# Kernel tuning notes

Measured on AMD Instinct MI355X. Metric: run time of the kernel, lower is better.

Reference implementation:

```python
import jax, jax.numpy as jnp
import numpy as np

HIDDEN = 1024
B, S = 4, 2048


def setup_inputs() -> dict:
    key = jax.random.key(0)
    ks = jax.random.split(key, 9)
    scale = 1.0 / np.sqrt(HIDDEN)
    mk = lambda k: (jax.random.normal(k, (HIDDEN, HIDDEN), dtype=jnp.float32) * scale)
    return {
        "x": jax.random.normal(ks[0], (B, S, HIDDEN), dtype=jnp.float32),
        "Wq": mk(ks[1]), "bq": jnp.zeros((HIDDEN,), jnp.float32),
        "Wk": mk(ks[2]), "bk": jnp.zeros((HIDDEN,), jnp.float32),
        "Wv": mk(ks[3]), "bv": jnp.zeros((HIDDEN,), jnp.float32),
        "Wo": mk(ks[4]), "bo": jnp.zeros((HIDDEN,), jnp.float32),
    }


def reference(x, Wq, bq, Wk, bk, Wv, bv, Wo, bo):
    # Single-head attention over the full hidden dim (num_heads unused in source).
    # Linear(H,H): y = x @ W^T + b ; weights stored [out,in] torch-style.
    q = jnp.einsum("bsh,oh->bso", x, Wq) + bq  # [B,S,H]
    k = jnp.einsum("bsh,oh->bso", x, Wk) + bk
    v = jnp.einsum("bsh,oh->bso", x, Wv) + bv
    scores = jnp.einsum("bqh,bkh->bqk", q, k) / jnp.sqrt(jnp.float32(HIDDEN))
    attn = jax.nn.softmax(scores, axis=-1)  # dropout rate is 0.0 (eval-equivalent)
    ctx = jnp.einsum("bqk,bkh->bqh", attn, v)
    return jnp.einsum("bsh,oh->bso", ctx, Wo) + bo
```

## Files before the change

### kernel.cpp

```cpp
#include <hip/hip_runtime.h>

#define HID 1024
#define SEQ 2048
#define NB 4
#define BS 8192

typedef __attribute__((ext_vector_type(8))) short short8;
typedef __attribute__((ext_vector_type(8))) unsigned short ushort8;
typedef __attribute__((ext_vector_type(4))) float f32x4;

__device__ __forceinline__ float bf2f(unsigned short u) {
  unsigned int x = ((unsigned int)u) << 16;
  return __builtin_bit_cast(float, x);
}
__device__ __forceinline__ unsigned short f2bf(float f) {
  unsigned int x = __builtin_bit_cast(unsigned int, f);
  x = x + 0x7fffu + ((x >> 16) & 1u);
  return (unsigned short)(x >> 16);
}

#define GLOAD16(g, l)                                                          \
  __builtin_amdgcn_global_load_lds(                                            \
      (const __attribute__((address_space(1))) unsigned int*)(g),              \
      (__attribute__((address_space(3))) unsigned int*)(l), 16, 0, 0)

__global__ void cast_f32_to_bf16(const float* __restrict__ in,
                                 unsigned short* __restrict__ out, int n) {
  int i = (blockIdx.x * 256 + threadIdx.x) * 8;
  if (i >= n) return;
  f32x4 a = *(const f32x4*)(in + i);
  f32x4 b = *(const f32x4*)(in + i + 4);
  ushort8 o;
  o[0] = f2bf(a[0]); o[1] = f2bf(a[1]); o[2] = f2bf(a[2]); o[3] = f2bf(a[3]);
  o[4] = f2bf(b[0]); o[5] = f2bf(b[1]); o[6] = f2bf(b[2]); o[7] = f2bf(b[3]);
  *(ushort8*)(out + i) = o;
}

__global__ __launch_bounds__(256) void transpose_cast(
    const float* __restrict__ in, unsigned short* __restrict__ out) {
  __shared__ float t[32][33];
  const int bx = blockIdx.x * 32, by = blockIdx.y * 32;
  const int tx = threadIdx.x & 31, ty = threadIdx.x >> 5;
#pragma unroll
  for (int i = 0; i < 4; ++i)
    t[ty + i * 8][tx] = in[(by + ty + i * 8) * 1024 + bx + tx];
  __syncthreads();
#pragma unroll
  for (int i = 0; i < 4; ++i)
    out[(bx + ty + i * 8) * 1024 + by + tx] = f2bf(t[tx][ty + i * 8]);
}

__global__ __launch_bounds__(256) void bias_fuse(const float* __restrict__ Wo,
                                                 const float* __restrict__ bv,
                                                 const float* __restrict__ bo,
                                                 float* __restrict__ bp) {
  const int row = blockIdx.x * 4 + (threadIdx.x >> 6);
  const int lane = threadIdx.x & 63;
  float s = 0.f;
  for (int k = lane; k < 1024; k += 64) s += Wo[row * 1024 + k] * bv[k];
#pragma unroll
  for (int off = 32; off >= 1; off >>= 1) s += __shfl_xor(s, off, 64);
  if (lane == 0) bp[row] = s + bo[row];
}

template <int BN, int OUT_F32, int BIAS_MODE, int EPI>
__global__ __launch_bounds__(256, 3) void gemm_tlp(
    const unsigned short* __restrict__ A, const unsigned short* __restrict__ B,
    void* __restrict__ Cv, const float* __restrict__ bias,
    const float* __restrict__ bias2, float* __restrict__ Srow, int K, int lda,
    int ldb, int ldc, long long bsA, long long bsB, long long bsC,
    float alpha) {
  static_assert(BN == 128 || BN == 64, "BN");
  constexpr int NF = BN / 32;
  constexpr int CB = BN / 64;

  __shared__ unsigned short lA[2][128 * 32];
  __shared__ unsigned short lB[2][BN * 32];

  const int tid = threadIdx.x;
  const int lane = tid & 63, wid = tid >> 6;
  const int fr = lane & 15, fq = lane >> 4;
  const int wm = wid >> 1, wn = wid & 1;

  const int nx = gridDim.x;
  const int nwg = nx * gridDim.y;
  int f = blockIdx.y * nx + blockIdx.x;
  f = (f & 7) * (nwg >> 3) + (f >> 3);
  const int bx = f % nx, by = f / nx;
  const int bz = blockIdx.z;

  const unsigned short* Ag = A + bz * bsA + (long long)by * 128 * lda;
  const unsigned short* Bg = B + bz * bsB + (long long)bx * BN * ldb;
  const int NT = K >> 5;

  const int srow = tid >> 2;
  const int scol = 8 * ((tid & 3) ^ ((tid >> 4) & 3));
  const int lbase = wid * 512;

  auto stageA = [&](int t) {
    unsigned short* d0 = &lA[t & 1][lbase];
    GLOAD16(Ag + (long long)srow * lda + t * 32 + scol, d0);
    GLOAD16(Ag + (long long)(64 + srow) * lda + t * 32 + scol, d0 + 2048);
  };
  auto stageB = [&](int t) {
    unsigned short* d0 = &lB[t & 1][lbase];
    GLOAD16(Bg + (long long)srow * ldb + t * 32 + scol, d0);
    if (CB == 2)
      GLOAD16(Bg + (long long)(64 + srow) * ldb + t * 32 + scol, d0 + 2048);
  };

  const int xm = ((fr >> 2) & 3) << 3;

  f32x4 acc[4][NF] = {};

  stageA(0);
  stageB(0);
  __syncthreads();

  for (int t = 0; t < NT; ++t) {
    if (t + 1 < NT) {
      stageA(t + 1);
      stageB(t + 1);
    }
    const unsigned short* pa = lA[t & 1];
    const unsigned short* pb = lB[t & 1];
    short8 av[4], bw[NF];
#pragma unroll
    for (int i = 0; i < 4; ++i)
      av[i] = *(const short8*)(pa +
                               (((wm * 64 + i * 16 + fr) * 32 + fq * 8) ^ xm));
#pragma unroll
    for (int n = 0; n < NF; ++n)
      bw[n] = *(const short8*)(pb + (((wn * (BN / 2) + n * 16 + fr) * 32 +
                                      fq * 8) ^ xm));
#pragma unroll
    for (int i = 0; i < 4; ++i)
#pragma unroll
      for (int n = 0; n < NF; ++n)
        acc[i][n] = __builtin_amdgcn_mfma_f32_16x16x32_bf16(av[i], bw[n],
                                                            acc[i][n], 0, 0, 0);
    __syncthreads();
  }

  const long long cb0 = (long long)bz * bsC;
  float* sredf = (float*)lA;
#pragma unroll
  for (int i = 0; i < 4; ++i)
#pragma unroll
    for (int j = 0; j < 4; ++j) {
      const int row = wm * 64 + i * 16 + fq * 4 + j;
      float inv = 1.0f;
      if (EPI == 2) inv = 1.0f / Srow[(long long)bz * SEQ + by * 128 + row];
      float rps = 0.0f;
#pragma unroll
      for (int n = 0; n < NF; ++n) {
        const int col = bx * BN + wn * (BN / 2) + n * 16 + fr;
        float v = acc[i][n][j] * alpha;
        if (EPI == 1) { v = __expf(v); rps += v; }
        if (EPI == 2) v *= inv;
        if (BIAS_MODE == 1) v += bias[col];
        if (BIAS_MODE == 3) v += (col < 1024) ? bias[col] : bias2[col - 1024];
        const long long idx = cb0 + (long long)(by * 128 + row) * ldc + col;
        if (OUT_F32)
          ((float*)Cv)[idx] = v;
        else
          ((unsigned short*)Cv)[idx] = f2bf(v);
      }
      if (EPI == 1) {
        rps += __shfl_xor(rps, 1, 64);
        rps += __shfl_xor(rps, 2, 64);
        rps += __shfl_xor(rps, 4, 64);
        rps += __shfl_xor(rps, 8, 64);
        if (fr == 0) sredf[row * 2 + wn] = rps;
      }
    }
  if (EPI == 1) {
    __syncthreads();
    if (tid < 128) {
      const float s2 = sredf[tid * 2] + sredf[tid * 2 + 1];
      atomicAdd(Srow + (long long)bz * SEQ + by * 128 + tid, s2);
    }
  }
}

extern "C" void kernel_launch(void* const* d_in, const int* in_sizes, int n_in,
                              void* d_out, int out_size, void* d_ws,
                              size_t ws_size, hipStream_t stream) {
  (void)in_sizes; (void)n_in; (void)out_size; (void)ws_size;
  const float* x = (const float*)d_in[0];
  const float* Wq = (const float*)d_in[1];
  const float* bq = (const float*)d_in[2];
  const float* Wk = (const float*)d_in[3];
  const float* bk = (const float*)d_in[4];
  const float* Wv = (const float*)d_in[5];
  const float* bv = (const float*)d_in[6];
  const float* Wo = (const float*)d_in[7];
  const float* bo = (const float*)d_in[8];
  float* out = (float*)d_out;

  char* ws = (char*)d_ws;
  unsigned short* xbf  = (unsigned short*)(ws + 0);
  unsigned short* wqk  = (unsigned short*)(ws + 16777216);
  unsigned short* wobf = (unsigned short*)(ws + 20971520);
  unsigned short* wvT  = (unsigned short*)(ws + 23068672);
  unsigned short* wov  = (unsigned short*)(ws + 25165824);
  float*          bpr  = (float*)        (ws + 27262976);
  float*          Srow = (float*)        (ws + 28311552);
  unsigned short* VWoT = (unsigned short*)(ws + 33554432);
  unsigned short* QKb  = (unsigned short*)(ws + 50331648);
  unsigned short* P    = (unsigned short*)(ws + 83886080);

  cast_f32_to_bf16<<<4096, 256, 0, stream>>>(x, xbf, BS * HID);
  cast_f32_to_bf16<<<512, 256, 0, stream>>>(Wq, wqk, HID * HID);
  cast_f32_to_bf16<<<512, 256, 0, stream>>>(Wk, wqk + HID * HID, HID * HID);
  cast_f32_to_bf16<<<512, 256, 0, stream>>>(Wo, wobf, HID * HID);
  transpose_cast<<<dim3(32, 32), 256, 0, stream>>>(Wv, wvT);
  bias_fuse<<<256, 256, 0, stream>>>(Wo, bv, bo, bpr);
  hipMemsetAsync(Srow, 0, NB * SEQ * sizeof(float), stream);

  gemm_tlp<128, 0, 0, 0><<<dim3(8, 8, 1), 256, 0, stream>>>(
      wobf, wvT, wov, nullptr, nullptr, nullptr, HID, HID, HID, HID, 0, 0, 0,
      1.0f);
  gemm_tlp<128, 0, 0, 0><<<dim3(64, 8, 1), 256, 0, stream>>>(
      wov, xbf, VWoT, nullptr, nullptr, nullptr, HID, HID, HID, BS, 0, 0, 0,
      1.0f);
  gemm_tlp<128, 0, 3, 0><<<dim3(16, 64, 1), 256, 0, stream>>>(
      xbf, wqk, QKb, bq, bk, nullptr, HID, HID, HID, 2048, 0, 0, 0, 1.0f);
  gemm_tlp<128, 0, 0, 1><<<dim3(16, 16, NB), 256, 0, stream>>>(
      QKb, QKb + 1024, P, nullptr, nullptr, Srow, HID, 2048, 2048, SEQ,
      (long long)SEQ * 2048, (long long)SEQ * 2048, (long long)SEQ * SEQ,
      0.03125f);
  gemm_tlp<128, 1, 1, 2><<<dim3(8, 16, NB), 256, 0, stream>>>(
      P, VWoT, out, bpr, nullptr, Srow, SEQ, SEQ, BS, HID,
      (long long)SEQ * SEQ, (long long)SEQ, (long long)SEQ * HID, 1.0f);
}
```

Baseline: 227.3 us.

## Switch GEMM to triple-buffered LDS pipeline with vmcnt waits and BN=64 variants

```diff
diff --git a/kernel.cpp b/kernel.cpp
--- a/kernel.cpp
+++ b/kernel.cpp
@@ -23,6 +23,11 @@
   __builtin_amdgcn_global_load_lds(                                            \
       (const __attribute__((address_space(1))) unsigned int*)(g),              \
       (__attribute__((address_space(3))) unsigned int*)(l), 16, 0, 0)
+
+template <int N>
+__device__ __forceinline__ void vmwait() {
+  asm volatile("s_waitcnt vmcnt(%0)" ::"i"(N) : "memory");
+}
 
 __global__ void cast_f32_to_bf16(const float* __restrict__ in,
                                  unsigned short* __restrict__ out, int n) {
@@ -64,7 +69,7 @@
 }
 
 template <int BN, int OUT_F32, int BIAS_MODE, int EPI>
-__global__ __launch_bounds__(256, 3) void gemm_tlp(
+__global__ __launch_bounds__(256, (BN == 128 ? 3 : 4)) void gemm_p3(
     const unsigned short* __restrict__ A, const unsigned short* __restrict__ B,
     void* __restrict__ Cv, const float* __restrict__ bias,
     const float* __restrict__ bias2, float* __restrict__ Srow, int K, int lda,
@@ -72,10 +77,10 @@
     float alpha) {
   static_assert(BN == 128 || BN == 64, "BN");
   constexpr int NF = BN / 32;
-  constexpr int CB = BN / 64;
-
-  __shared__ unsigned short lA[2][128 * 32];
-  __shared__ unsigned short lB[2][BN * 32];
+  constexpr int LPS = (BN == 128) ? 4 : 3;
+
+  __shared__ unsigned short lA[3][128 * 32];
+  __shared__ unsigned short lB[3][BN * 32];
 
   const int tid = threadIdx.x;
   const int lane = tid & 63, wid = tid >> 6;
@@ -94,36 +99,35 @@
   const int NT = K >> 5;
 
   const int srow = tid >> 2;
-  const int scol = 8 * ((tid & 3) ^ ((tid >> 4) & 3));
+  const int scol = 8 * ((tid & 3) ^ ((tid >> 3) & 3));
   const int lbase = wid * 512;
 
-  auto stageA = [&](int t) {
-    unsigned short* d0 = &lA[t & 1][lbase];
-    GLOAD16(Ag + (long long)srow * lda + t * 32 + scol, d0);
-    GLOAD16(Ag + (long long)(64 + srow) * lda + t * 32 + scol, d0 + 2048);
+  auto stage = [&](int t) {
+    const int b3 = t - (t / 3) * 3;
+    unsigned short* dA = &lA[b3][lbase];
+    GLOAD16(Ag + (long long)srow * lda + t * 32 + scol, dA);
+    GLOAD16(Ag + (long long)(64 + srow) * lda + t * 32 + scol, dA + 2048);
+    unsigned short* dB = &lB[b3][lbase];
+    GLOAD16(Bg + (long long)srow * ldb + t * 32 + scol, dB);
+    if (BN == 128)
+      GLOAD16(Bg + (long long)(64 + srow) * ldb + t * 32 + scol, dB + 2048);
   };
-  auto stageB = [&](int t) {
-    unsigned short* d0 = &lB[t & 1][lbase];
-    GLOAD16(Bg + (long long)srow * ldb + t * 32 + scol, d0);
-    if (CB == 2)
-      GLOAD16(Bg + (long long)(64 + srow) * ldb + t * 32 + scol, d0 + 2048);
-  };
-
-  const int xm = ((fr >> 2) & 3) << 3;
+
+  const int xm = ((fr >> 1) & 3) << 3;
 
   f32x4 acc[4][NF] = {};
 
-  stageA(0);
-  stageB(0);
-  __syncthreads();
+  stage(0);
+  stage(1);
 
   for (int t = 0; t < NT; ++t) {
-    if (t + 1 < NT) {
-      stageA(t + 1);
-      stageB(t + 1);
-    }
-    const unsigned short* pa = lA[t & 1];
-    const unsigned short* pb = lB[t & 1];
+    if (t + 1 < NT) vmwait<LPS>(); else vmwait<0>();
+    __builtin_amdgcn_s_barrier();
+    __builtin_amdgcn_sched_barrier(0);
+    if (t + 2 < NT) stage(t + 2);
+    const int b3 = t - (t / 3) * 3;
+    const unsigned short* pa = lA[b3];
+    const unsigned short* pb = lB[b3];
     short8 av[4], bw[NF];
 #pragma unroll
     for (int i = 0; i < 4; ++i)
@@ -139,9 +143,9 @@
       for (int n = 0; n < NF; ++n)
         acc[i][n] = __builtin_amdgcn_mfma_f32_16x16x32_bf16(av[i], bw[n],
                                                             acc[i][n], 0, 0, 0);
-    __syncthreads();
   }
 
+  if (EPI == 1) __syncthreads();
   const long long cb0 = (long long)bz * bsC;
   float* sredf = (float*)lA;
 #pragma unroll
@@ -218,19 +222,19 @@
   bias_fuse<<<256, 256, 0, stream>>>(Wo, bv, bo, bpr);
   hipMemsetAsync(Srow, 0, NB * SEQ * sizeof(float), stream);
 
-  gemm_tlp<128, 0, 0, 0><<<dim3(8, 8, 1), 256, 0, stream>>>(
+  gemm_p3<128, 0, 0, 0><<<dim3(8, 8, 1), 256, 0, stream>>>(
       wobf, wvT, wov, nullptr, nullptr, nullptr, HID, HID, HID, HID, 0, 0, 0,
       1.0f);
-  gemm_tlp<128, 0, 0, 0><<<dim3(64, 8, 1), 256, 0, stream>>>(
+  gemm_p3<64, 0, 0, 0><<<dim3(128, 8, 1), 256, 0, stream>>>(
       wov, xbf, VWoT, nullptr, nullptr, nullptr, HID, HID, HID, BS, 0, 0, 0,
       1.0f);
-  gemm_tlp<128, 0, 3, 0><<<dim3(16, 64, 1), 256, 0, stream>>>(
+  gemm_p3<128, 0, 3, 0><<<dim3(16, 64, 1), 256, 0, stream>>>(
       xbf, wqk, QKb, bq, bk, nullptr, HID, HID, HID, 2048, 0, 0, 0, 1.0f);
-  gemm_tlp<128, 0, 0, 1><<<dim3(16, 16, NB), 256, 0, stream>>>(
+  gemm_p3<128, 0, 0, 1><<<dim3(16, 16, NB), 256, 0, stream>>>(
       QKb, QKb + 1024, P, nullptr, nullptr, Srow, HID, 2048, 2048, SEQ,
       (long long)SEQ * 2048, (long long)SEQ * 2048, (long long)SEQ * SEQ,
       0.03125f);
-  gemm_tlp<128, 1, 1, 2><<<dim3(8, 16, NB), 256, 0, stream>>>(
+  gemm_p3<64, 1, 1, 2><<<dim3(16, 16, NB), 256, 0, stream>>>(
       P, VWoT, out, bpr, nullptr, Srow, SEQ, SEQ, BS, HID,
       (long long)SEQ * SEQ, (long long)SEQ, (long long)SEQ * HID, 1.0f);
 }
```

After: 251.3 us. 10.6% more time.

## Unroll GEMM main loop by two with static LDS buffers and BN=64 tiles

Applied to the files above, without the earlier changes.

```diff
diff --git a/kernel.cpp b/kernel.cpp
--- a/kernel.cpp
+++ b/kernel.cpp
@@ -64,7 +64,7 @@
 }
 
 template <int BN, int OUT_F32, int BIAS_MODE, int EPI>
-__global__ __launch_bounds__(256, 3) void gemm_tlp(
+__global__ __launch_bounds__(256, (BN == 128 ? 3 : 4)) void gemm_b(
     const unsigned short* __restrict__ A, const unsigned short* __restrict__ B,
     void* __restrict__ Cv, const float* __restrict__ bias,
     const float* __restrict__ bias2, float* __restrict__ Srow, int K, int lda,
@@ -72,7 +72,6 @@
     float alpha) {
   static_assert(BN == 128 || BN == 64, "BN");
   constexpr int NF = BN / 32;
-  constexpr int CB = BN / 64;
 
   __shared__ unsigned short lA[2][128 * 32];
   __shared__ unsigned short lB[2][BN * 32];
@@ -94,36 +93,26 @@
   const int NT = K >> 5;
 
   const int srow = tid >> 2;
-  const int scol = 8 * ((tid & 3) ^ ((tid >> 4) & 3));
+  const int scol = 8 * ((tid & 3) ^ ((tid >> 3) & 3));
   const int lbase = wid * 512;
 
-  auto stageA = [&](int t) {
-    unsigned short* d0 = &lA[t & 1][lbase];
-    GLOAD16(Ag + (long long)srow * lda + t * 32 + scol, d0);
-    GLOAD16(Ag + (long long)(64 + srow) * lda + t * 32 + scol, d0 + 2048);
+  auto stageA = [&](int t, int b) {
+    unsigned short* d = &lA[b][lbase];
+    GLOAD16(Ag + (long long)srow * lda + t * 32 + scol, d);
+    GLOAD16(Ag + (long long)(64 + srow) * lda + t * 32 + scol, d + 2048);
   };
-  auto stageB = [&](int t) {
-    unsigned short* d0 = &lB[t & 1][lbase];
-    GLOAD16(Bg + (long long)srow * ldb + t * 32 + scol, d0);
-    if (CB == 2)
-      GLOAD16(Bg + (long long)(64 + srow) * ldb + t * 32 + scol, d0 + 2048);
+  auto stageB = [&](int t, int b) {
+    unsigned short* d = &lB[b][lbase];
+    GLOAD16(Bg + (long long)srow * ldb + t * 32 + scol, d);
+    if (BN == 128)
+      GLOAD16(Bg + (long long)(64 + srow) * ldb + t * 32 + scol, d + 2048);
   };
 
-  const int xm = ((fr >> 2) & 3) << 3;
+  const int xm = ((fr >> 1) & 3) << 3;
 
   f32x4 acc[4][NF] = {};
 
-  stageA(0);
-  stageB(0);
-  __syncthreads();
-
-  for (int t = 0; t < NT; ++t) {
-    if (t + 1 < NT) {
-      stageA(t + 1);
-      stageB(t + 1);
-    }
-    const unsigned short* pa = lA[t & 1];
-    const unsigned short* pb = lB[t & 1];
+  auto compute = [&](const unsigned short* pa, const unsigned short* pb) {
     short8 av[4], bw[NF];
 #pragma unroll
     for (int i = 0; i < 4; ++i)
@@ -133,12 +122,30 @@
     for (int n = 0; n < NF; ++n)
       bw[n] = *(const short8*)(pb + (((wn * (BN / 2) + n * 16 + fr) * 32 +
                                       fq * 8) ^ xm));
+    asm volatile("s_waitcnt lgkmcnt(0)" ::: "memory");
+    __builtin_amdgcn_sched_barrier(0);
 #pragma unroll
     for (int i = 0; i < 4; ++i)
 #pragma unroll
       for (int n = 0; n < NF; ++n)
         acc[i][n] = __builtin_amdgcn_mfma_f32_16x16x32_bf16(av[i], bw[n],
                                                             acc[i][n], 0, 0, 0);
+  };
+
+  stageA(0, 0);
+  stageB(0, 0);
+  __syncthreads();
+
+  for (int t = 0; t < NT; t += 2) {
+    stageA(t + 1, 1);
+    stageB(t + 1, 1);
+    compute(lA[0], lB[0]);
+    __syncthreads();
+    if (t + 2 < NT) {
+      stageA(t + 2, 0);
+      stageB(t + 2, 0);
+    }
+    compute(lA[1], lB[1]);
     __syncthreads();
   }
 
@@ -218,19 +225,19 @@
   bias_fuse<<<256, 256, 0, stream>>>(Wo, bv, bo, bpr);
   hipMemsetAsync(Srow, 0, NB * SEQ * sizeof(float), stream);
 
-  gemm_tlp<128, 0, 0, 0><<<dim3(8, 8, 1), 256, 0, stream>>>(
+  gemm_b<128, 0, 0, 0><<<dim3(8, 8, 1), 256, 0, stream>>>(
       wobf, wvT, wov, nullptr, nullptr, nullptr, HID, HID, HID, HID, 0, 0, 0,
       1.0f);
-  gemm_tlp<128, 0, 0, 0><<<dim3(64, 8, 1), 256, 0, stream>>>(
+  gemm_b<64, 0, 0, 0><<<dim3(128, 8, 1), 256, 0, stream>>>(
       wov, xbf, VWoT, nullptr, nullptr, nullptr, HID, HID, HID, BS, 0, 0, 0,
       1.0f);
-  gemm_tlp<128, 0, 3, 0><<<dim3(16, 64, 1), 256, 0, stream>>>(
+  gemm_b<128, 0, 3, 0><<<dim3(16, 64, 1), 256, 0, stream>>>(
       xbf, wqk, QKb, bq, bk, nullptr, HID, HID, HID, 2048, 0, 0, 0, 1.0f);
-  gemm_tlp<128, 0, 0, 1><<<dim3(16, 16, NB), 256, 0, stream>>>(
+  gemm_b<128, 0, 0, 1><<<dim3(16, 16, NB), 256, 0, stream>>>(
       QKb, QKb + 1024, P, nullptr, nullptr, Srow, HID, 2048, 2048, SEQ,
       (long long)SEQ * 2048, (long long)SEQ * 2048, (long long)SEQ * SEQ,
       0.03125f);
-  gemm_tlp<128, 1, 1, 2><<<dim3(8, 16, NB), 256, 0, stream>>>(
+  gemm_b<64, 1, 1, 2><<<dim3(16, 16, NB), 256, 0, stream>>>(
       P, VWoT, out, bpr, nullptr, Srow, SEQ, SEQ, BS, HID,
       (long long)SEQ * SEQ, (long long)SEQ, (long long)SEQ * HID, 1.0f);
 }
```

Measured after the change: 245.0 us. 7.8% more time.
